# Kernel tuning notes

Measured on AMD Instinct MI355X. Metric: run time of the kernel, lower is better.

The kernel has to match this reference:

```python
import jax, jax.numpy as jnp
import numpy as np
from math import factorial

# ---- module hyperparameters (from init_kwargs) ----
SPECIES = np.array([1, 6, 7, 8], np.int32)
LOW, HIGH, NG, RSWITCH, W, LMAX = 0.0, 6.0, 20, 1.0, 2.0, 2
LWEIGHTS = np.array([1.0, 1.0, 1.0], np.float32)
INVF = [2.0, 2.0, 2.0]


def _angular_tables():
    comps, weights, idx, inv = [], [], [], []
    for i in range(LMAX + 1):
        for k in range(i + 1):
            for m in range(i - k + 1):
                n = i - k - m
                comps.append([n, m, k])
                weights.append(factorial(i) / (factorial(n) * factorial(m) * factorial(k)))
                idx.append(i)
                inv.append(INVF[i])
    return (np.array(comps, np.int32), np.array(weights, np.float32),
            np.array(idx, np.int32), np.array(inv, np.float32))

COMPS, ANGW, ANGIDX, INVFACT = _angular_tables()   # 10 angular components for lmax=2
OFFSETS = np.linspace(LOW, HIGH, NG + 1, dtype=np.float32)[1:]
SQRTPI = np.float32(np.sqrt(np.pi))
NSP = len(SPECIES)
COMBOS = [(i, j) for i in range(NSP) for j in range(i + 1, NSP)]
NMBODY = NSP + len(COMBOS)
FPSIZE = NG * (LMAX + 1) * NMBODY


def _int_pow(x, e):
    # e in {0,1,2}; avoids NaN from pow(negative_base, float_exponent)
    return jnp.where(e == 0, jnp.ones_like(x), jnp.where(e == 1, x, x * x))


def _forward(coordinates, nuclear_charges, natom_counts, neighbours):
    B, N, _ = coordinates.shape
    mask = neighbours >= 0                              # padded slots are -1
    nb = jnp.maximum(neighbours, 0)                     # safe_fill
    bidx = jnp.arange(B)[:, None, None]
    local = coordinates[bidx, nb]                       # [B,N,M,3] neighbour gather
    nbh = coordinates[:, :, None, :] - local
    nbh = jnp.where(mask[..., None], nbh, 1.0)          # keep padded slots finite
    d = jnp.linalg.norm(nbh, axis=3)                    # [B,N,M]
    coeff = mask.astype(coordinates.dtype)
    nbr_z = nuclear_charges[bidx, nb]                   # [B,N,M]

    dsw = (d - RSWITCH) / (HIGH - RSWITCH)
    cut = 1.0 - 6.0 * dsw**5 + 15.0 * dsw**4 - 10.0 * dsw**3
    d2 = d * d
    sigma2 = jnp.log(1.0 + W / d2)
    mu = jnp.log(d / jnp.sqrt(1.0 + W / d2))
    off = jnp.asarray(OFFSETS)
    centered = (jnp.log(off) - mu[..., None]) ** 2      # [B,N,M,G]
    s2 = sigma2[..., None]
    radial = (1.0 / (off * jnp.sqrt(s2) * SQRTPI)) * jnp.exp(-centered / (2.0 * s2)) \
             * cut[..., None] * coeff[..., None]        # [B,N,M,G]

    expo = jnp.asarray(INVFACT + ANGIDX.astype(np.float32))
    inv_scaling = (1.0 / d[..., None]) ** expo * coeff[..., None]   # [B,N,M,A]
    comps = jnp.asarray(COMPS)
    angular = inv_scaling \
        * _int_pow(nbh[..., None, 0], comps[:, 0]) \
        * _int_pow(nbh[..., None, 1], comps[:, 1]) \
        * _int_pow(nbh[..., None, 2], comps[:, 2])      # [B,N,M,A]

    angw = jnp.asarray(ANGW)
    lw = jnp.asarray(LWEIGHTS)
    onehot = jnp.asarray((ANGIDX[:, None] == np.arange(LMAX + 1)[None, :]).astype(np.float32))

    sp_masks = [(nbr_z == int(z)).astype(coordinates.dtype) for z in SPECIES]

    def group_fp(gmask):
        ang = angular * gmask[..., None]
        t = jnp.einsum('bnma,bnmg->bnag', ang, radial)          # sum over neighbours
        orb = angw[None, None, :, None] * (t * t)               # [B,N,A,G]
        elem = jnp.einsum('bnag,al->bnlg', orb, onehot)         # index_add over l
        return lw[None, None, :, None] * elem                   # [B,N,L+1,G]

    fps = [group_fp(m) for m in sp_masks]
    for (i, j) in COMBOS:
        gmask = jnp.maximum(sp_masks[i], sp_masks[j])
        fps.append(group_fp(gmask) - (fps[i] + fps[j]))

    fp = jnp.stack(fps, axis=3)                                 # [B,N,L+1,NMBODY,G]
    atom_mask = (jnp.arange(N)[None, :] < natom_counts[:, None]).astype(coordinates.dtype)
    fp = fp * atom_mask[:, :, None, None, None]
    return fp.reshape(B, N, FPSIZE)


def setup_inputs() -> dict:
    rng = np.random.default_rng(0)
    B, N, M = 128, 128, 64
    box = 13.5
    coords = rng.uniform(0.0, box, (B, N, 3)).astype(np.float32)
    charges = rng.choice(np.array([1, 6, 7, 8], np.int32), size=(B, N)).astype(np.int32)
    counts = rng.integers(96, N + 1, B).astype(np.int32)
    diff = coords[:, :, None, :] - coords[:, None, :, :]
    dist = np.linalg.norm(diff, axis=-1)
    exist = np.arange(N)[None, :] < counts[:, None]
    valid = (dist < HIGH) & (dist > 1e-6) & exist[:, :, None] & exist[:, None, :]
    order = np.argsort(~valid, axis=2, kind='stable')[:, :, :M]
    vmask = np.take_along_axis(valid, order, axis=2)
    neighbours = np.where(vmask, order, -1).astype(np.int32)
    return {
        "coordinates": jnp.asarray(coords),
        "nuclear_charges": jnp.asarray(charges),
        "natom_counts": jnp.asarray(counts),
        "neighbours": jnp.asarray(neighbours),
    }


def reference(coordinates, nuclear_charges, natom_counts, neighbours):
    return _forward(coordinates, nuclear_charges, natom_counts, neighbours)
```

## Files before the change

### kernel.cpp

```cpp
#include <hip/hip_runtime.h>


#define B_   128
#define N_   128
#define M_   64
#define NG_  20
#define NSP_ 4
#define FPSIZE_ 600
#define APB  16
#define NTASK (APB * M_)
#define BLOCK_THREADS (APB * NG_)
#define SLOTS 81

__global__ __launch_bounds__(BLOCK_THREADS)
void gto_fp_kernel(const float* __restrict__ coords,
                   const int*   __restrict__ charges,
                   const int*   __restrict__ counts,
                   const int*   __restrict__ neigh,
                   float*       __restrict__ out)
{
    __shared__ float4 sP[APB][SLOTS];
    __shared__ float2 sQ[APB][SLOTS];
    __shared__ int s_cnt[APB][NSP_];
    __shared__ int s_pc[APB][NSP_];
    __shared__ int s_start[APB][NSP_];
    __shared__ int s_pos[APB][NSP_];

    const int tid = threadIdx.x;
    const int blockBase = blockIdx.x * APB;
    const int bidx = blockBase / N_;

    if (tid < APB * NSP_) ((int*)s_cnt)[tid] = 0;
    __syncthreads();

    for (int t = tid; t < NTASK; t += BLOCK_THREADS) {
        const int la = t >> 6, m = t & 63;
        const int nb = neigh[(blockBase + la) * M_ + m];
        if (nb >= 0) {
            const int z = charges[bidx * N_ + nb];
            const int s = (z == 1) ? 0 : (z - 5);
            atomicAdd(&s_cnt[la][s], 1);
        }
    }
    __syncthreads();

    if (tid < APB) {
        int st = 0;
#pragma unroll
        for (int s = 0; s < NSP_; ++s) {
            const int c  = s_cnt[tid][s];
            const int pc = (c + 3) & ~3;
            s_pc[tid][s]    = pc;
            s_start[tid][s] = st;
            s_pos[tid][s]   = st;
            st += pc;
        }
    }
    __syncthreads();

    for (int t = tid; t < NTASK; t += BLOCK_THREADS) {
        const int la = t >> 6, m = t & 63;
        const int atom = blockBase + la;
        const int nb = neigh[atom * M_ + m];
        if (nb < 0) continue;
        const int nidx = bidx * N_ + nb;
        const float dx = coords[atom * 3 + 0] - coords[nidx * 3 + 0];
        const float dy = coords[atom * 3 + 1] - coords[nidx * 3 + 1];
        const float dz = coords[atom * 3 + 2] - coords[nidx * 3 + 2];
        const int   z  = charges[nidx];

        const float d2     = dx * dx + dy * dy + dz * dz;
        const float inv_d  = __builtin_amdgcn_rsqf(d2);
        const float d      = d2 * inv_d;
        const float inv_d2 = inv_d * inv_d;

        const float dsw  = (d - 1.0f) * 0.2f;
        const float dsw2 = dsw * dsw;
        const float cut  = 1.0f - dsw2 * dsw * fmaf(6.0f, dsw2, fmaf(-15.0f, dsw, 10.0f));

        const float sigma2 = __logf(fmaf(2.0f, inv_d2, 1.0f));
        const float mu     = 0.5f * (__logf(d2) - sigma2);
        const float amp    = fmaxf(__builtin_amdgcn_rsqf(sigma2) * cut * inv_d2,
                                   1.0e-30f);

        const float F   = -0.72134752f * __builtin_amdgcn_rcpf(sigma2);
        const float Fm  = F * mu;
        const float c2v = fmaf(Fm, mu, __log2f(amp));

        const int s = (z == 1) ? 0 : (z - 5);
        const int slot = atomicAdd(&s_pos[la][s], 1);
        sP[la][slot] = make_float4(F, -(Fm + Fm), c2v, dx * inv_d);
        sQ[la][slot] = make_float2(dy * inv_d, dz * inv_d);
    }

    if (tid < APB * NSP_) {
        const int la = tid >> 2, s = tid & 3;
        const int st = s_start[la][s];
        const int c  = s_cnt[la][s];
        const int pc = s_pc[la][s];
        for (int k = st + c; k < st + pc; ++k) {
            sP[la][k] = make_float4(0.0f, 0.0f, -200.0f, 0.0f);
            sQ[la][k] = make_float2(0.0f, 0.0f);
        }
    }
    __syncthreads();

    const int g  = tid % NG_;
    const int la = tid / NG_;
    const int atom = blockBase + la;
    const int n = atom % N_;

    const float off = 0.3f * (float)(g + 1);
    const float lo  = __logf(off);
    const float lo2 = lo * lo;
    const float inv_off_spi = 1.0f / (off * 1.7724538509055159f);

    float T[NSP_][10];
#pragma unroll
    for (int s = 0; s < NSP_; ++s)
#pragma unroll
        for (int a = 0; a < 10; ++a) T[s][a] = 0.0f;

#define BODY(SS, P, Q)                                                        \
    {                                                                         \
        const float rad = __builtin_amdgcn_exp2f(                             \
            fmaf(P.x, lo2, fmaf(P.y, lo, P.z)));                              \
        const float rx = rad * P.w, ry = rad * Q.x, rz = rad * Q.y;           \
        T[SS][0] += rad;                                                      \
        T[SS][1] += rx;  T[SS][2] += ry;  T[SS][3] += rz;                     \
        T[SS][4] = fmaf(rx, P.w, T[SS][4]);                                   \
        T[SS][5] = fmaf(rx, Q.x, T[SS][5]);                                   \
        T[SS][6] = fmaf(ry, Q.x, T[SS][6]);                                   \
        T[SS][7] = fmaf(rx, Q.y, T[SS][7]);                                   \
        T[SS][8] = fmaf(ry, Q.y, T[SS][8]);                                   \
        T[SS][9] = fmaf(rz, Q.y, T[SS][9]);                                   \
    }

#define ACC(SS)                                                               \
    {                                                                         \
        const int e0 = s_start[la][SS];                                       \
        const int e1 = e0 + s_pc[la][SS];    \
        for (int m = e0; m < e1; m += 4) {                                    \
            const float4 Pa = sP[la][m + 0]; const float2 Qa = sQ[la][m + 0]; \
            const float4 Pb = sP[la][m + 1]; const float2 Qb = sQ[la][m + 1]; \
            const float4 Pc = sP[la][m + 2]; const float2 Qc = sQ[la][m + 2]; \
            const float4 Pd = sP[la][m + 3]; const float2 Qd = sQ[la][m + 3]; \
            BODY(SS, Pa, Qa)                                                  \
            BODY(SS, Pb, Qb)                                                  \
            BODY(SS, Pc, Qc)                                                  \
            BODY(SS, Pd, Qd)                                                  \
        }                                                                     \
    }
    ACC(0) ACC(1) ACC(2) ACC(3)
#undef ACC
#undef BODY

    const float amask = (n < counts[bidx]) ? 1.0f : 0.0f;
    const float scale = amask * inv_off_spi * inv_off_spi;
    float* op = out + atom * FPSIZE_ + g;

#pragma unroll
    for (int l = 0; l < 3; ++l) {
        const int a0 = (l == 0) ? 0 : (l == 1) ? 1 : 4;
        const int a1 = (l == 0) ? 1 : (l == 1) ? 4 : 10;
#pragma unroll
        for (int s = 0; s < NSP_; ++s) {
            float v = 0.0f;
#pragma unroll
            for (int a = a0; a < a1; ++a) {
                const float w = (a == 5 || a == 7 || a == 8) ? 2.0f : 1.0f;
                v = fmaf(w * T[s][a], T[s][a], v);
            }
            op[(l * 10 + s) * NG_] = scale * v;
        }
        int mb = 4;
#pragma unroll
        for (int i = 0; i < NSP_; ++i) {
#pragma unroll
            for (int j = i + 1; j < NSP_; ++j) {
                float v = 0.0f;
#pragma unroll
                for (int a = a0; a < a1; ++a) {
                    const float w = (a == 5 || a == 7 || a == 8) ? 2.0f : 1.0f;
                    v = fmaf(w * T[i][a], T[j][a], v);
                }
                op[(l * 10 + mb) * NG_] = scale * (2.0f * v);
                ++mb;
            }
        }
    }
}

extern "C" void kernel_launch(void* const* d_in, const int* in_sizes, int n_in,
                              void* d_out, int out_size, void* d_ws, size_t ws_size,
                              hipStream_t stream) {
    const float* coords  = (const float*)d_in[0];
    const int*   charges = (const int*)d_in[1];
    const int*   counts  = (const int*)d_in[2];
    const int*   neigh   = (const int*)d_in[3];
    float*       outp    = (float*)d_out;

    const int blocks = (B_ * N_) / APB;
    gto_fp_kernel<<<blocks, BLOCK_THREADS, 0, stream>>>(coords, charges, counts, neigh, outp);
}
```

Before: 87.70 us.

## Replace shared-memory atomic bucketing with wave ballot compaction per atom

```diff
diff --git a/kernel.cpp b/kernel.cpp
--- a/kernel.cpp
+++ b/kernel.cpp
@@ -8,9 +8,8 @@
 #define NSP_ 4
 #define FPSIZE_ 600
 #define APB  16
-#define NTASK (APB * M_)
 #define BLOCK_THREADS (APB * NG_)
-#define SLOTS 81
+#define NWAVES 5
 
 __global__ __launch_bounds__(BLOCK_THREADS)
 void gto_fp_kernel(const float* __restrict__ coords,
@@ -19,51 +18,23 @@
                    const int*   __restrict__ neigh,
                    float*       __restrict__ out)
 {
-    __shared__ float4 sP[APB][SLOTS];
-    __shared__ float2 sQ[APB][SLOTS];
+    __shared__ float4 sP[APB][M_ + 1];
+    __shared__ float2 sQ[APB][M_ + 1];
     __shared__ int s_cnt[APB][NSP_];
-    __shared__ int s_pc[APB][NSP_];
     __shared__ int s_start[APB][NSP_];
-    __shared__ int s_pos[APB][NSP_];
 
-    const int tid = threadIdx.x;
+    const int tid  = threadIdx.x;
+    const int wave = tid >> 6;
+    const int lane = tid & 63;
     const int blockBase = blockIdx.x * APB;
     const int bidx = blockBase / N_;
 
-    if (tid < APB * NSP_) ((int*)s_cnt)[tid] = 0;
-    __syncthreads();
+    for (int la = wave; la < APB; la += NWAVES) {
+        const int atom = blockBase + la;
+        const int nb = neigh[atom * M_ + lane];
+        const bool valid = (nb >= 0);
+        const int nidx = bidx * N_ + (valid ? nb : 0);
 
-    for (int t = tid; t < NTASK; t += BLOCK_THREADS) {
-        const int la = t >> 6, m = t & 63;
-        const int nb = neigh[(blockBase + la) * M_ + m];
-        if (nb >= 0) {
-            const int z = charges[bidx * N_ + nb];
-            const int s = (z == 1) ? 0 : (z - 5);
-            atomicAdd(&s_cnt[la][s], 1);
-        }
-    }
-    __syncthreads();
-
-    if (tid < APB) {
-        int st = 0;
-#pragma unroll
-        for (int s = 0; s < NSP_; ++s) {
-            const int c  = s_cnt[tid][s];
-            const int pc = (c + 3) & ~3;
-            s_pc[tid][s]    = pc;
-            s_start[tid][s] = st;
-            s_pos[tid][s]   = st;
-            st += pc;
-        }
-    }
-    __syncthreads();
-
-    for (int t = tid; t < NTASK; t += BLOCK_THREADS) {
-        const int la = t >> 6, m = t & 63;
-        const int atom = blockBase + la;
-        const int nb = neigh[atom * M_ + m];
-        if (nb < 0) continue;
-        const int nidx = bidx * N_ + nb;
         const float dx = coords[atom * 3 + 0] - coords[nidx * 3 + 0];
         const float dy = coords[atom * 3 + 1] - coords[nidx * 3 + 1];
         const float dz = coords[atom * 3 + 2] - coords[nidx * 3 + 2];
@@ -88,19 +59,30 @@
         const float c2v = fmaf(Fm, mu, __log2f(amp));
 
         const int s = (z == 1) ? 0 : (z - 5);
-        const int slot = atomicAdd(&s_pos[la][s], 1);
-        sP[la][slot] = make_float4(F, -(Fm + Fm), c2v, dx * inv_d);
-        sQ[la][slot] = make_float2(dy * inv_d, dz * inv_d);
-    }
 
-    if (tid < APB * NSP_) {
-        const int la = tid >> 2, s = tid & 3;
-        const int st = s_start[la][s];
-        const int c  = s_cnt[la][s];
-        const int pc = s_pc[la][s];
-        for (int k = st + c; k < st + pc; ++k) {
-            sP[la][k] = make_float4(0.0f, 0.0f, -200.0f, 0.0f);
-            sQ[la][k] = make_float2(0.0f, 0.0f);
+        const unsigned long long m0 = __ballot(valid && s == 0);
+        const unsigned long long m1 = __ballot(valid && s == 1);
+        const unsigned long long m2 = __ballot(valid && s == 2);
+        const unsigned long long m3 = __ballot(valid && s == 3);
+        const int c0 = __popcll(m0), c1 = __popcll(m1), c2 = __popcll(m2);
+        const unsigned long long below = (lane == 63) ? ~0ULL >> 1
+                                                      : (1ULL << lane) - 1ULL;
+        if (valid) {
+            int slot;
+            if      (s == 0) slot = __popcll(m0 & below);
+            else if (s == 1) slot = c0 + __popcll(m1 & below);
+            else if (s == 2) slot = c0 + c1 + __popcll(m2 & below);
+            else             slot = c0 + c1 + c2 + __popcll(m3 & below);
+            sP[la][slot] = make_float4(F, -(Fm + Fm), c2v, dx * inv_d);
+            sQ[la][slot] = make_float2(dy * inv_d, dz * inv_d);
+        }
+        if (lane == 0) {
+            s_cnt[la][0] = c0; s_cnt[la][1] = c1;
+            s_cnt[la][2] = c2; s_cnt[la][3] = __popcll(m3);
+            s_start[la][0] = 0;
+            s_start[la][1] = c0;
+            s_start[la][2] = c0 + c1;
+            s_start[la][3] = c0 + c1 + c2;
         }
     }
     __syncthreads();
@@ -139,16 +121,17 @@
 #define ACC(SS)                                                               \
     {                                                                         \
         const int e0 = s_start[la][SS];                                       \
-        const int e1 = e0 + s_pc[la][SS];    \
-        for (int m = e0; m < e1; m += 4) {                                    \
-            const float4 Pa = sP[la][m + 0]; const float2 Qa = sQ[la][m + 0]; \
+        const int e1 = e0 + s_cnt[la][SS];                                    \
+        int m = e0;                                                           \
+        for (; m + 1 < e1; m += 2) {                                          \
+            const float4 Pa = sP[la][m];     const float2 Qa = sQ[la][m];     \
             const float4 Pb = sP[la][m + 1]; const float2 Qb = sQ[la][m + 1]; \
-            const float4 Pc = sP[la][m + 2]; const float2 Qc = sQ[la][m + 2]; \
-            const float4 Pd = sP[la][m + 3]; const float2 Qd = sQ[la][m + 3]; \
             BODY(SS, Pa, Qa)                                                  \
             BODY(SS, Pb, Qb)                                                  \
-            BODY(SS, Pc, Qc)                                                  \
-            BODY(SS, Pd, Qd)                                                  \
+        }                                                                     \
+        if (m < e1) {                                                         \
+            const float4 Pa = sP[la][m]; const float2 Qa = sQ[la][m];         \
+            BODY(SS, Pa, Qa)                                                  \
         }                                                                     \
     }
     ACC(0) ACC(1) ACC(2) ACC(3)
```

Measured after the change: 85.08 us. -3.0%, faster.
